# Kernel tuning notes

Hardware: AMD Instinct MI355X
Metric: run time of the kernel (lower is better)

The kernel has to match this reference:

```python
import jax, jax.numpy as jnp
import numpy as np

N_NODES = 50000
D = 256
N_EDGES = 262144
N_LAYER = 3
EPS = 1e-5


def setup_inputs() -> dict:
    key = jax.random.key(0)
    ks = jax.random.split(key, 8)
    x = jax.random.normal(ks[0], (N_NODES, D), dtype=jnp.float32)
    jg_edge_index = jax.random.randint(ks[1], (2, N_EDGES), 0, N_NODES, dtype=jnp.int64)
    ln_w = jnp.ones((D,), dtype=jnp.float32)
    # torch Linear weight is [out, in]; stack per-layer weights [L, D, D]
    Ws = jax.random.normal(ks[2], (N_LAYER, D, D), dtype=jnp.float32) * (1.0 / np.sqrt(D))
    gammas = jnp.ones((N_LAYER, D), dtype=jnp.float32)
    betas = jnp.zeros((N_LAYER, D), dtype=jnp.float32)
    W_out = jax.random.normal(ks[3], (1, D), dtype=jnp.float32) * (1.0 / np.sqrt(D))
    return {"x": x, "jg_edge_index": jg_edge_index, "ln_w": ln_w,
            "Ws": Ws, "gammas": gammas, "betas": betas, "W_out": W_out}


def reference(x, jg_edge_index, ln_w, Ws, gammas, betas, W_out):
    src, dst = jg_edge_index[0], jg_edge_index[1]
    # edge features: gather + add -> [E, D]
    h = x[src, :] + x[dst, :]
    # LayerNorm over feature dim, weight only (bias=False), eps=1e-5
    mu = jnp.mean(h, axis=-1, keepdims=True)
    var = jnp.mean(jnp.square(h - mu), axis=-1, keepdims=True)
    h = (h - mu) * jax.lax.rsqrt(var + EPS) * ln_w
    # projection blocks: Linear (no bias) -> BatchNorm1d (training stats) -> ReLU
    for i in range(N_LAYER):
        h = h @ Ws[i].T  # [E, D]
        bmu = jnp.mean(h, axis=0)                      # batch mean over edges
        bvar = jnp.mean(jnp.square(h - bmu), axis=0)   # biased batch var
        h = (h - bmu) * jax.lax.rsqrt(bvar + EPS) * gammas[i] + betas[i]
        h = jax.nn.relu(h)
    logits = (h @ W_out.T).squeeze(-1)  # [E]
    return logits
```

## Files before the change

### kernel.cpp

```cpp
#include <hip/hip_runtime.h>
#include <hip/hip_bf16.h>

#define NEDGE 262144
#define DIM 256
#define NLAYER 3
#define EPSV 1e-5f

#define GBM 512
#define RC 64
#define NCH (GBM / RC)
#define GEMM_GRID (NEDGE / GBM)

typedef __attribute__((ext_vector_type(8))) short bf16x8_t;
typedef __attribute__((ext_vector_type(4))) float f32x4_t;

__device__ __forceinline__ float bf2f(short s) {
  unsigned u = ((unsigned)(unsigned short)s) << 16;
  return __builtin_bit_cast(float, u);
}
__device__ __forceinline__ short f2bf(float f) {
  __hip_bfloat16 h = __float2bfloat16(f);
  return __builtin_bit_cast(short, h);
}

extern "C" __global__ void __launch_bounds__(256)
k_cvt(const float* __restrict__ src, short* __restrict__ dst, int n) {
  int i = blockIdx.x * 256 + threadIdx.x;
  if (i < n) dst[i] = f2bf(src[i]);
}

extern "C" __global__ void __launch_bounds__(512)
k_gemm1f(const float* __restrict__ x, const int* __restrict__ ei,
         const float* __restrict__ lnw, const short* __restrict__ W,
         short* __restrict__ C, float* __restrict__ psum, float* __restrict__ psq) {
  __shared__ short As[2][RC * DIM];
  __shared__ int sIdx[GBM], dIdx[GBM];
  const int tid = threadIdx.x;
  const int w = tid >> 6;
  const int lane = tid & 63;
  const int rl = lane & 15;
  const int kh = lane >> 4;
  const int row0 = blockIdx.x * GBM;
  const int colbase = w * 32;
  const int cst = tid & 31;

  sIdx[tid] = ei[row0 + tid];
  dIdx[tid] = ei[NEDGE + row0 + tid];

  bf16x8_t wf[2][8];
#pragma unroll
  for (int n = 0; n < 2; ++n)
#pragma unroll
    for (int ks = 0; ks < 8; ++ks)
      wf[n][ks] = *(const bf16x8_t*)(W + (size_t)(colbase + n * 16 + rl) * DIM + ks * 32 + kh * 8);

  float lw[8];
#pragma unroll
  for (int j = 0; j < 8; ++j) lw[j] = lnw[cst * 8 + j];

  float st_s0 = 0.f, st_s1 = 0.f, st_q0 = 0.f, st_q1 = 0.f;
  float4 rs0[4], rs1[4], rd0[4], rd1[4];

  auto ldgather = [&](int t) {
#pragma unroll
    for (int i = 0; i < 4; ++i) {
      const int r = (tid >> 5) + 16 * i;
      const int s = sIdx[t * RC + r];
      const int d = dIdx[t * RC + r];
      const float* ps = x + (size_t)s * DIM + cst * 8;
      const float* pd = x + (size_t)d * DIM + cst * 8;
      rs0[i] = *(const float4*)ps;
      rs1[i] = *(const float4*)(ps + 4);
      rd0[i] = *(const float4*)pd;
      rd1[i] = *(const float4*)(pd + 4);
    }
  };

  auto lnwrite = [&](int b) {
#pragma unroll
    for (int i = 0; i < 4; ++i) {
      const int r = (tid >> 5) + 16 * i;
      float v[8];
      v[0] = rs0[i].x + rd0[i].x; v[1] = rs0[i].y + rd0[i].y;
      v[2] = rs0[i].z + rd0[i].z; v[3] = rs0[i].w + rd0[i].w;
      v[4] = rs1[i].x + rd1[i].x; v[5] = rs1[i].y + rd1[i].y;
      v[6] = rs1[i].z + rd1[i].z; v[7] = rs1[i].w + rd1[i].w;
      float s = 0.f, ss = 0.f;
#pragma unroll
      for (int j = 0; j < 8; ++j) { s += v[j]; ss = fmaf(v[j], v[j], ss); }
#pragma unroll
      for (int off = 16; off >= 1; off >>= 1) {
        s += __shfl_xor(s, off);
        ss += __shfl_xor(ss, off);
      }
      const float mu = s * (1.0f / DIM);
      const float var = ss * (1.0f / DIM) - mu * mu;
      const float sc = rsqrtf(var + EPSV);
      bf16x8_t o;
#pragma unroll
      for (int j = 0; j < 8; ++j) o[j] = f2bf((v[j] - mu) * sc * lw[j]);
      *(bf16x8_t*)(&As[b][r * DIM + ((cst ^ (r & 7)) << 3)]) = o;
    }
  };

  auto compute = [&](int t, int b) {
    const f32x4_t zero = {0.f, 0.f, 0.f, 0.f};
    f32x4_t acc[4][2];
#pragma unroll
    for (int m = 0; m < 4; ++m) { acc[m][0] = zero; acc[m][1] = zero; }
    const short* base = As[b];
#pragma unroll
    for (int ks = 0; ks < 8; ++ks) {
      bf16x8_t af[4];
#pragma unroll
      for (int m = 0; m < 4; ++m) {
        const int row = m * 16 + rl;
        const int c = ks * 4 + kh;
        af[m] = *(const bf16x8_t*)(base + row * DIM + ((c ^ (row & 7)) << 3));
      }
#pragma unroll
      for (int m = 0; m < 4; ++m) {
        acc[m][0] = __builtin_amdgcn_mfma_f32_16x16x32_bf16(af[m], wf[0][ks], acc[m][0], 0, 0, 0);
        acc[m][1] = __builtin_amdgcn_mfma_f32_16x16x32_bf16(af[m], wf[1][ks], acc[m][1], 0, 0, 0);
      }
    }
    const int rquad = kh << 2;
#pragma unroll
    for (int n = 0; n < 2; ++n) {
      const int col = colbase + n * 16 + rl;
      float s = 0.f, q = 0.f;
#pragma unroll
      for (int m = 0; m < 4; ++m) {
        const size_t rb = (size_t)(row0 + t * RC + m * 16 + rquad) * DIM + col;
#pragma unroll
        for (int r = 0; r < 4; ++r) {
          const float f = acc[m][n][r];
          C[rb + (size_t)r * DIM] = f2bf(f);
          s += f;
          q = fmaf(f, f, q);
        }
      }
      if (n == 0) { st_s0 += s; st_q0 += q; }
      else        { st_s1 += s; st_q1 += q; }
    }
  };

  __syncthreads();
  ldgather(0);
  lnwrite(0);
  __syncthreads();
  for (int t = 0; t < NCH; ++t) {
    if (t + 1 < NCH) ldgather(t + 1);
    compute(t, t & 1);
    if (t + 1 < NCH) lnwrite((t + 1) & 1);
    __syncthreads();
  }

  {
    float s = st_s0, q = st_q0;
    s += __shfl_xor(s, 16); s += __shfl_xor(s, 32);
    q += __shfl_xor(q, 16); q += __shfl_xor(q, 32);
    if (lane < 16) {
      psum[(size_t)blockIdx.x * DIM + colbase + rl] = s;
      psq [(size_t)blockIdx.x * DIM + colbase + rl] = q;
    }
  }
  {
    float s = st_s1, q = st_q1;
    s += __shfl_xor(s, 16); s += __shfl_xor(s, 32);
    q += __shfl_xor(q, 16); q += __shfl_xor(q, 32);
    if (lane < 16) {
      psum[(size_t)blockIdx.x * DIM + colbase + 16 + rl] = s;
      psq [(size_t)blockIdx.x * DIM + colbase + 16 + rl] = q;
    }
  }
}

extern "C" __global__ void __launch_bounds__(512, 2)
k_gemm_bn(const short* __restrict__ A, const short* __restrict__ W,
          short* __restrict__ C, float* __restrict__ psum, float* __restrict__ psq,
          const float* __restrict__ bsc, const float* __restrict__ bsh) {
  __shared__ short As[2][RC * DIM];
  const int tid = threadIdx.x;
  const int w = tid >> 6;
  const int lane = tid & 63;
  const int rl = lane & 15;
  const int kh = lane >> 4;
  const int row0 = blockIdx.x * GBM;
  const int colbase = w * 32;

  bf16x8_t wf[2][8];
#pragma unroll
  for (int n = 0; n < 2; ++n)
#pragma unroll
    for (int ks = 0; ks < 8; ++ks)
      wf[n][ks] = *(const bf16x8_t*)(W + (size_t)(colbase + n * 16 + rl) * DIM + ks * 32 + kh * 8);

  const int cst = tid & 31;
  float sc0[8], sh0[8];
#pragma unroll
  for (int j = 0; j < 8; ++j) {
    sc0[j] = bsc[cst * 8 + j];
    sh0[j] = bsh[cst * 8 + j];
  }

  float st_s0 = 0.f, st_s1 = 0.f, st_q0 = 0.f, st_q1 = 0.f;

  auto ldreg = [&](int t, bf16x8_t* r) {
#pragma unroll
    for (int i = 0; i < 4; ++i) {
      const int row = (tid + i * 512) >> 5;
      r[i] = *(const bf16x8_t*)(A + (size_t)(row0 + t * RC + row) * DIM + cst * 8);
    }
  };
  auto xform_write = [&](int b, bf16x8_t* r) {
#pragma unroll
    for (int i = 0; i < 4; ++i) {
      const int row = (tid + i * 512) >> 5;
      bf16x8_t v = r[i];
      bf16x8_t o;
#pragma unroll
      for (int j = 0; j < 8; ++j)
        o[j] = f2bf(fmaxf(fmaf(bf2f(v[j]), sc0[j], sh0[j]), 0.0f));
      *(bf16x8_t*)(&As[b][row * DIM + ((cst ^ (row & 7)) << 3)]) = o;
    }
  };

  auto compute = [&](int t, int b) {
    const f32x4_t zero = {0.f, 0.f, 0.f, 0.f};
    f32x4_t acc[4][2];
#pragma unroll
    for (int m = 0; m < 4; ++m) { acc[m][0] = zero; acc[m][1] = zero; }
    const short* base = As[b];
#pragma unroll
    for (int ks = 0; ks < 8; ++ks) {
      bf16x8_t af[4];
#pragma unroll
      for (int m = 0; m < 4; ++m) {
        const int row = m * 16 + rl;
        const int c = ks * 4 + kh;
        af[m] = *(const bf16x8_t*)(base + row * DIM + ((c ^ (row & 7)) << 3));
      }
#pragma unroll
      for (int m = 0; m < 4; ++m) {
        acc[m][0] = __builtin_amdgcn_mfma_f32_16x16x32_bf16(af[m], wf[0][ks], acc[m][0], 0, 0, 0);
        acc[m][1] = __builtin_amdgcn_mfma_f32_16x16x32_bf16(af[m], wf[1][ks], acc[m][1], 0, 0, 0);
      }
    }
    const int rquad = kh << 2;
#pragma unroll
    for (int n = 0; n < 2; ++n) {
      const int col = colbase + n * 16 + rl;
      float s = 0.f, q = 0.f;
#pragma unroll
      for (int m = 0; m < 4; ++m) {
        const size_t rb = (size_t)(row0 + t * RC + m * 16 + rquad) * DIM + col;
#pragma unroll
        for (int r = 0; r < 4; ++r) {
          const float f = acc[m][n][r];
          C[rb + (size_t)r * DIM] = f2bf(f);
          s += f;
          q = fmaf(f, f, q);
        }
      }
      if (n == 0) { st_s0 += s; st_q0 += q; }
      else        { st_s1 += s; st_q1 += q; }
    }
  };

  bf16x8_t ra[4], rb[4];
  ldreg(0, ra);
  xform_write(0, ra);
  ldreg(1, rb);
  __syncthreads();
  for (int t = 0; t < NCH; ++t) {
    if (t + 2 < NCH) ldreg(t + 2, ra);
    compute(t, t & 1);
    if (t + 1 < NCH) xform_write((t + 1) & 1, rb);
    __syncthreads();
#pragma unroll
    for (int i = 0; i < 4; ++i) { bf16x8_t tmp = ra[i]; ra[i] = rb[i]; rb[i] = tmp; }
  }

  {
    float s = st_s0, q = st_q0;
    s += __shfl_xor(s, 16); s += __shfl_xor(s, 32);
    q += __shfl_xor(q, 16); q += __shfl_xor(q, 32);
    if (lane < 16) {
      psum[(size_t)blockIdx.x * DIM + colbase + rl] = s;
      psq [(size_t)blockIdx.x * DIM + colbase + rl] = q;
    }
  }
  {
    float s = st_s1, q = st_q1;
    s += __shfl_xor(s, 16); s += __shfl_xor(s, 32);
    q += __shfl_xor(q, 16); q += __shfl_xor(q, 32);
    if (lane < 16) {
      psum[(size_t)blockIdx.x * DIM + colbase + 16 + rl] = s;
      psq [(size_t)blockIdx.x * DIM + colbase + 16 + rl] = q;
    }
  }
}

extern "C" __global__ void __launch_bounds__(64)
k_stats(const float* __restrict__ psum, const float* __restrict__ psq,
        const float* __restrict__ gamma, const float* __restrict__ beta,
        float* __restrict__ sc, float* __restrict__ sh, int nblk) {
  const int c = blockIdx.x;
  const int lane = threadIdx.x;
  float s = 0.0f, q = 0.0f;
  for (int b = lane; b < nblk; b += 64) {
    s += psum[(size_t)b * DIM + c];
    q += psq[(size_t)b * DIM + c];
  }
#pragma unroll
  for (int off = 32; off >= 1; off >>= 1) {
    s += __shfl_xor(s, off);
    q += __shfl_xor(q, off);
  }
  if (lane == 0) {
    const float inv = 1.0f / NEDGE;
    const float mu = s * inv;
    const float var = q * inv - mu * mu;
    const float scale = rsqrtf(var + EPSV) * gamma[c];
    sc[c] = scale;
    sh[c] = beta[c] - mu * scale;
  }
}

extern "C" __global__ void __launch_bounds__(256)
k_head(const short* __restrict__ h3, const float* __restrict__ sc,
       const float* __restrict__ sh, const float* __restrict__ wout,
       float* __restrict__ out) {
  const int e = (blockIdx.x << 3) + (threadIdx.x >> 5);
  const int g = threadIdx.x & 31;
  const int c = g * 8;
  const bf16x8_t v = *(const bf16x8_t*)(h3 + (size_t)e * DIM + c);
  float acc = 0.f;
#pragma unroll
  for (int j = 0; j < 8; ++j)
    acc += fmaxf(fmaf(bf2f(v[j]), sc[c + j], sh[c + j]), 0.0f) * wout[c + j];
#pragma unroll
  for (int off = 16; off >= 1; off >>= 1) acc += __shfl_xor(acc, off);
  if (g == 0) out[e] = acc;
}

extern "C" void kernel_launch(void* const* d_in, const int* in_sizes, int n_in,
                              void* d_out, int out_size, void* d_ws, size_t ws_size,
                              hipStream_t stream) {
  const float* x = (const float*)d_in[0];
  const int* ei = (const int*)d_in[1];
  const float* lnw = (const float*)d_in[2];
  const float* Ws = (const float*)d_in[3];
  const float* gammas = (const float*)d_in[4];
  const float* betas = (const float*)d_in[5];
  const float* wout = (const float*)d_in[6];
  float* out = (float*)d_out;

  char* ws = (char*)d_ws;
  const size_t HBYTES = (size_t)NEDGE * DIM * 2;
  short* h = (short*)ws;
  short* Wb = (short*)(ws + HBYTES);
  char* p = ws + HBYTES + (size_t)NLAYER * DIM * DIM * 2;
  float* psum = (float*)p;
  float* psq = psum + (size_t)GEMM_GRID * DIM;
  float* bnsc = psq + (size_t)GEMM_GRID * DIM;
  float* bnsh = bnsc + NLAYER * DIM;

  k_cvt<<<(NLAYER * DIM * DIM + 255) / 256, 256, 0, stream>>>(Ws, Wb, NLAYER * DIM * DIM);

  k_gemm1f<<<GEMM_GRID, 512, 0, stream>>>(x, ei, lnw, Wb, h, psum, psq);
  k_stats<<<DIM, 64, 0, stream>>>(psum, psq, gammas, betas, bnsc, bnsh, GEMM_GRID);

  for (int l = 1; l < NLAYER; ++l) {
    k_gemm_bn<<<GEMM_GRID, 512, 0, stream>>>(h, Wb + (size_t)l * DIM * DIM, h,
                                             psum, psq,
                                             bnsc + (size_t)(l - 1) * DIM,
                                             bnsh + (size_t)(l - 1) * DIM);
    k_stats<<<DIM, 64, 0, stream>>>(psum, psq, gammas + (size_t)l * DIM,
                                    betas + (size_t)l * DIM,
                                    bnsc + (size_t)l * DIM, bnsh + (size_t)l * DIM,
                                    GEMM_GRID);
  }
  k_head<<<NEDGE / 8, 256, 0, stream>>>(h, bnsc + (size_t)(NLAYER - 1) * DIM,
                                        bnsh + (size_t)(NLAYER - 1) * DIM, wout, out);
}
```

Before: 267.4 us.

## Pre-convert node features to bf16 and deepen gather prefetch to two chunks

Adds a kernel that converts the node feature table x to bf16 once, so the first fused GEMM gathers half as many bytes per edge row. The gather pipeline now keeps two register buffers, loading chunk t+2/t+3 while earlier chunks are computed, to hide more gather latency. In exchange it adds an extra conversion pass over the 50k x 256 table, rounds LayerNorm inputs to bf16 before the sum (a small precision change), and raises register pressure.

After: 259.6 us. -2.9%, faster.

```diff
diff --git a/kernel.cpp b/kernel.cpp
--- a/kernel.cpp
+++ b/kernel.cpp
@@ -3,6 +3,7 @@
 
 #define NEDGE 262144
 #define DIM 256
+#define NNODE 50000
 #define NLAYER 3
 #define EPSV 1e-5f
 
@@ -29,8 +30,20 @@
   if (i < n) dst[i] = f2bf(src[i]);
 }
 
+extern "C" __global__ void __launch_bounds__(256)
+k_cvt_x(const float* __restrict__ src, short* __restrict__ dst, int n8) {
+  int i = blockIdx.x * 256 + threadIdx.x;
+  if (i >= n8) return;
+  const float4 a = *(const float4*)(src + (size_t)i * 8);
+  const float4 b = *(const float4*)(src + (size_t)i * 8 + 4);
+  bf16x8_t o;
+  o[0] = f2bf(a.x); o[1] = f2bf(a.y); o[2] = f2bf(a.z); o[3] = f2bf(a.w);
+  o[4] = f2bf(b.x); o[5] = f2bf(b.y); o[6] = f2bf(b.z); o[7] = f2bf(b.w);
+  *(bf16x8_t*)(dst + (size_t)i * 8) = o;
+}
+
 extern "C" __global__ void __launch_bounds__(512)
-k_gemm1f(const float* __restrict__ x, const int* __restrict__ ei,
+k_gemm1f(const short* __restrict__ xb, const int* __restrict__ ei,
          const float* __restrict__ lnw, const short* __restrict__ W,
          short* __restrict__ C, float* __restrict__ psum, float* __restrict__ psq) {
   __shared__ short As[2][RC * DIM];
@@ -59,32 +72,37 @@
   for (int j = 0; j < 8; ++j) lw[j] = lnw[cst * 8 + j];
 
   float st_s0 = 0.f, st_s1 = 0.f, st_q0 = 0.f, st_q1 = 0.f;
-  float4 rs0[4], rs1[4], rd0[4], rd1[4];
-
-  auto ldgather = [&](int t) {
+
+  bf16x8_t rsA[4], rdA[4], rsB[4], rdB[4];
+
+  auto ldgA = [&](int t) {
 #pragma unroll
     for (int i = 0; i < 4; ++i) {
       const int r = (tid >> 5) + 16 * i;
       const int s = sIdx[t * RC + r];
       const int d = dIdx[t * RC + r];
-      const float* ps = x + (size_t)s * DIM + cst * 8;
-      const float* pd = x + (size_t)d * DIM + cst * 8;
-      rs0[i] = *(const float4*)ps;
-      rs1[i] = *(const float4*)(ps + 4);
-      rd0[i] = *(const float4*)pd;
-      rd1[i] = *(const float4*)(pd + 4);
-    }
-  };
-
-  auto lnwrite = [&](int b) {
+      rsA[i] = *(const bf16x8_t*)(xb + (size_t)s * DIM + cst * 8);
+      rdA[i] = *(const bf16x8_t*)(xb + (size_t)d * DIM + cst * 8);
+    }
+  };
+  auto ldgB = [&](int t) {
+#pragma unroll
+    for (int i = 0; i < 4; ++i) {
+      const int r = (tid >> 5) + 16 * i;
+      const int s = sIdx[t * RC + r];
+      const int d = dIdx[t * RC + r];
+      rsB[i] = *(const bf16x8_t*)(xb + (size_t)s * DIM + cst * 8);
+      rdB[i] = *(const bf16x8_t*)(xb + (size_t)d * DIM + cst * 8);
+    }
+  };
+
+  auto lnwr = [&](int b, bf16x8_t* rs, bf16x8_t* rd) {
 #pragma unroll
     for (int i = 0; i < 4; ++i) {
       const int r = (tid >> 5) + 16 * i;
       float v[8];
-      v[0] = rs0[i].x + rd0[i].x; v[1] = rs0[i].y + rd0[i].y;
-      v[2] = rs0[i].z + rd0[i].z; v[3] = rs0[i].w + rd0[i].w;
-      v[4] = rs1[i].x + rd1[i].x; v[5] = rs1[i].y + rd1[i].y;
-      v[6] = rs1[i].z + rd1[i].z; v[7] = rs1[i].w + rd1[i].w;
+#pragma unroll
+      for (int j = 0; j < 8; ++j) v[j] = bf2f(rs[i][j]) + bf2f(rd[i][j]);
       float s = 0.f, ss = 0.f;
 #pragma unroll
       for (int j = 0; j < 8; ++j) { s += v[j]; ss = fmaf(v[j], v[j], ss); }
@@ -146,13 +164,18 @@
   };
 
   __syncthreads();
-  ldgather(0);
-  lnwrite(0);
+  ldgA(0);
+  ldgB(1);
+  lnwr(0, rsA, rdA);
   __syncthreads();
-  for (int t = 0; t < NCH; ++t) {
-    if (t + 1 < NCH) ldgather(t + 1);
-    compute(t, t & 1);
-    if (t + 1 < NCH) lnwrite((t + 1) & 1);
+  for (int t = 0; t < NCH; t += 2) {
+    if (t + 2 < NCH) ldgA(t + 2);
+    compute(t, 0);
+    lnwr(1, rsB, rdB);
+    __syncthreads();
+    if (t + 3 < NCH) ldgB(t + 3);
+    compute(t + 1, 1);
+    if (t + 2 < NCH) lnwr(0, rsA, rdA);
     __syncthreads();
   }
 
@@ -366,10 +389,12 @@
   float* psq = psum + (size_t)GEMM_GRID * DIM;
   float* bnsc = psq + (size_t)GEMM_GRID * DIM;
   float* bnsh = bnsc + NLAYER * DIM;
+  short* xb = (short*)(bnsh + NLAYER * DIM);
 
   k_cvt<<<(NLAYER * DIM * DIM + 255) / 256, 256, 0, stream>>>(Ws, Wb, NLAYER * DIM * DIM);
-
-  k_gemm1f<<<GEMM_GRID, 512, 0, stream>>>(x, ei, lnw, Wb, h, psum, psq);
+  k_cvt_x<<<(NNODE * DIM / 8 + 255) / 256, 256, 0, stream>>>(x, xb, NNODE * DIM / 8);
+
+  k_gemm1f<<<GEMM_GRID, 512, 0, stream>>>(xb, ei, lnw, Wb, h, psum, psq);
   k_stats<<<DIM, 64, 0, stream>>>(psum, psq, gammas, betas, bnsc, bnsh, GEMM_GRID);
 
   for (int l = 1; l < NLAYER; ++l) {
```
